# Kernel optimization log

Measured on AMD Instinct MI355X. Metric: run time of the kernel, lower is better.

Reference implementation:

```python
import jax, jax.numpy as jnp
import numpy as np

D_HIDDEN = 1024
NUM_HEADS = 16
D_HEAD = D_HIDDEN // NUM_HEADS


def setup_inputs() -> dict:
    key = jax.random.key(0)
    ks = jax.random.split(key, 9)
    N, S, D = 4, 2048, D_HIDDEN
    s = 1.0 / np.sqrt(D)
    inp = {
        "x": jax.random.normal(ks[0], (N, S, D), dtype=jnp.float32),
        "Wq": jax.random.uniform(ks[1], (D, D), jnp.float32, -s, s),
        "bq": jnp.zeros((D,), jnp.float32),
        "Wk": jax.random.uniform(ks[2], (D, D), jnp.float32, -s, s),
        "bk": jnp.zeros((D,), jnp.float32),
        "Wv": jax.random.uniform(ks[3], (D, D), jnp.float32, -s, s),
        "bv": jnp.zeros((D,), jnp.float32),
        "Wo": jax.random.uniform(ks[4], (D, D), jnp.float32, -s, s),
        "bo": jnp.zeros((D,), jnp.float32),
        "ln_gamma": jnp.ones((D,), jnp.float32),
        "ln_beta": jnp.zeros((D,), jnp.float32),
    }
    return inp


def _layer_norm(x, gamma, beta, eps=1e-5):
    mu = jnp.mean(x, axis=-1, keepdims=True)
    var = jnp.var(x, axis=-1, keepdims=True)
    return (x - mu) * jax.lax.rsqrt(var + eps) * gamma + beta


def reference(x, Wq, bq, Wk, bk, Wv, bv, Wo, bo, ln_gamma, ln_beta):
    N, S, D = x.shape
    H, Dh = NUM_HEADS, D_HEAD
    xn = _layer_norm(x, ln_gamma, ln_beta)
    # torch Linear: y = x @ W.T + b
    q = (xn @ Wq.T + bq).reshape(N, S, H, Dh)
    k = (xn @ Wk.T + bk).reshape(N, S, H, Dh)
    v = (xn @ Wv.T + bv).reshape(N, S, H, Dh)
    # scores: [N, H, S, S]
    scores = jnp.einsum('nxhd,nyhd->nhxy', q, k) / np.sqrt(Dh)
    # causal mask: positions y > x get -inf
    mask = jnp.triu(jnp.full((S, S), -jnp.inf, dtype=scores.dtype), k=1)
    attn = jax.nn.softmax(scores + mask[None, None], axis=-1)
    z = jnp.einsum('nhxy,nyhd->nxhd', attn, v).reshape(N, S, D)
    return z @ Wo.T + bo
```

## Files before the change

### kernel.cpp

```cpp
#include <hip/hip_runtime.h>

typedef unsigned short u16;
typedef unsigned int   u32;
typedef __bf16 bf16x8 __attribute__((ext_vector_type(8)));
typedef float  f32x4  __attribute__((ext_vector_type(4)));
typedef unsigned short u16x8 __attribute__((ext_vector_type(8)));
typedef unsigned short u16x4 __attribute__((ext_vector_type(4)));

#define SEQ 2048
#define DM  1024
#define TOKS 8388608
#define SCLQ 0.18033688f

__device__ __forceinline__ float bf2f(u16 u) {
    u32 i = ((u32)u) << 16;
    float f; __builtin_memcpy(&f, &i, 4); return f;
}
__device__ __forceinline__ u16 f2bf(float f) {
    u32 i; __builtin_memcpy(&i, &f, 4);
    return (u16)((i + 0x7FFFu + ((i >> 16) & 1u)) >> 16);
}
__device__ __forceinline__ bf16x8 ld8(const u16* p) {
    return __builtin_bit_cast(bf16x8, *(const u16x8*)p);
}
#define GLD16(src, dst) __builtin_amdgcn_global_load_lds( \
    (const __attribute__((address_space(1))) void*)(src), \
    (__attribute__((address_space(3))) void*)(dst), 16, 0, 0)

__global__ __launch_bounds__(64) void detect_k(const u32* __restrict__ x, int* __restrict__ flag) {
    const int lane = threadIdx.x;
    u32 w = x[lane];
    int e0 = (int)((w >> 7) & 0xFFu);
    int cnt = (e0 >= 100 && e0 <= 140) ? 1 : 0;
#pragma unroll
    for (int off = 32; off; off >>= 1) cnt += __shfl_xor(cnt, off);
    if (lane == 0) *flag = (cnt < 32) ? 1 : 0;
}

__global__ __launch_bounds__(256) void convert_k(const void* s0, const void* s1, const void* s2, const void* s3,
                                                 const void* v0, const void* v1, const void* v2, const void* v3,
                                                 const void* v4, const void* v5,
                                                 u16* __restrict__ dstW, u16* __restrict__ dstV,
                                                 const int* __restrict__ flagp) {
    const int y = blockIdx.y, tid = threadIdx.x;
    const int fp32m = *flagp;
    const void* src; u16* dst; size_t off;
    if (y < 4) {
        src = (y == 0) ? s0 : (y == 1) ? s1 : (y == 2) ? s2 : s3;
        dst = dstW + (size_t)y * 1048576;
        off = (size_t)blockIdx.x * 1024 + tid * 4;
    } else {
        const int i = blockIdx.x;
        if (i >= 6) return;
        src = (i == 0) ? v0 : (i == 1) ? v1 : (i == 2) ? v2 : (i == 3) ? v3 : (i == 4) ? v4 : v5;
        dst = dstV + (size_t)i * 1024;
        off = (size_t)tid * 4;
    }
    u16x4 o;
    if (fp32m) {
        const float* f = (const float*)src + off;
#pragma unroll
        for (int j = 0; j < 4; ++j) o[j] = f2bf(f[j]);
    } else {
        o = *(const u16x4*)((const u16*)src + off);
    }
    *(u16x4*)(dst + off) = o;
}

__global__ __launch_bounds__(256) void ln_k(const void* __restrict__ xv,
                                            const u16* __restrict__ g,
                                            const u16* __restrict__ b,
                                            u16* __restrict__ xn,
                                            const int* __restrict__ flagp) {
    const int row = blockIdx.x, tid = threadIdx.x;
    const int fp32m = *flagp;
    float f[4], s1 = 0.f, s2 = 0.f;
    if (fp32m) {
        f32x4 v = *(const f32x4*)((const float*)xv + (size_t)row * DM + tid * 4);
#pragma unroll
        for (int j = 0; j < 4; ++j) f[j] = v[j];
    } else {
        u16x4 v = *(const u16x4*)((const u16*)xv + (size_t)row * DM + tid * 4);
#pragma unroll
        for (int j = 0; j < 4; ++j) f[j] = bf2f(v[j]);
    }
#pragma unroll
    for (int j = 0; j < 4; ++j) { s1 += f[j]; s2 += f[j] * f[j]; }
#pragma unroll
    for (int off = 32; off; off >>= 1) { s1 += __shfl_xor(s1, off); s2 += __shfl_xor(s2, off); }
    __shared__ float red[8];
    const int wave = tid >> 6, lane = tid & 63;
    if (lane == 0) { red[wave] = s1; red[4 + wave] = s2; }
    __syncthreads();
    s1 = red[0] + red[1] + red[2] + red[3];
    s2 = red[4] + red[5] + red[6] + red[7];
    const float mu = s1 * (1.f / DM);
    const float var = s2 * (1.f / DM) - mu * mu;
    const float rs = rsqrtf(var + 1e-5f);
    u16x4 gv = *(const u16x4*)(g + tid * 4);
    u16x4 bv = *(const u16x4*)(b + tid * 4);
    u16x4 o;
#pragma unroll
    for (int j = 0; j < 4; ++j) o[j] = f2bf((f[j] - mu) * rs * bf2f(gv[j]) + bf2f(bv[j]));
    *(u16x4*)(xn + (size_t)row * DM + tid * 4) = o;
}

template <int VT>
__device__ __forceinline__ void gemm_core(u16* As, u16* Bs,
                                          const u16* __restrict__ A,
                                          const u16* __restrict__ W,
                                          const u16* __restrict__ bias,
                                          u16* __restrict__ out,
                                          const int* __restrict__ flagp,
                                          float scale) {
    const int tid = threadIdx.x, wave = tid >> 6, lane = tid & 63;
    const int l4 = lane & 15, q4 = lane >> 4;
    const int bm = blockIdx.x, bn = blockIdx.y;
    const int wm = (wave >> 1) * 64, wn = (wave & 1) * 64;
    int fp32m = 0;
    if (VT == 2) fp32m = *flagp;
    f32x4 acc[4][4] = {};
    const int srow = wave * 32 + (lane >> 2);
    const int skoff = (lane & 3) * 8;
    const u16* Ag = A + ((size_t)(bm * 128 + srow)) * DM + skoff;
    const u16* Wg = W + ((size_t)(bn * 128 + srow)) * DM + skoff;
    u16* As0 = As + wave * 1024;
    u16* Bs0 = Bs + wave * 1024;

    for (int k0 = 0; k0 < DM; k0 += 32) {
        GLD16(Ag + k0, As0);
        GLD16(Ag + 16 * DM + k0, As0 + 512);
        GLD16(Wg + k0, Bs0);
        GLD16(Wg + 16 * DM + k0, Bs0 + 512);
        __syncthreads();
        bf16x8 af[4], bfr[4];
#pragma unroll
        for (int t = 0; t < 4; ++t)
            af[t] = ld8(As + (wm + t * 16 + l4) * 32 + q4 * 8);
#pragma unroll
        for (int t = 0; t < 4; ++t)
            bfr[t] = ld8(Bs + (wn + t * 16 + l4) * 32 + q4 * 8);
#pragma unroll
        for (int mt = 0; mt < 4; ++mt)
#pragma unroll
            for (int nt = 0; nt < 4; ++nt)
                acc[mt][nt] = __builtin_amdgcn_mfma_f32_16x16x32_bf16(af[mt], bfr[nt], acc[mt][nt], 0, 0, 0);
        __syncthreads();
    }

#pragma unroll
    for (int nt = 0; nt < 4; ++nt) {
        const int col = bn * 128 + wn + nt * 16 + l4;
        const float bs = bf2f(bias[col]);
#pragma unroll
        for (int mt = 0; mt < 4; ++mt) {
            const int row0 = bm * 128 + wm + mt * 16 + q4 * 4;
            if (VT == 1) {
                const int nb = row0 >> 11, s0 = row0 & 2047;
                u16x4 pk;
#pragma unroll
                for (int r = 0; r < 4; ++r) pk[r] = f2bf((acc[mt][nt][r] + bs) * scale);
                *(u16x4*)(out + ((size_t)(nb * 1024 + col)) * SEQ + s0) = pk;
            } else if (VT == 2 && fp32m) {
#pragma unroll
                for (int r = 0; r < 4; ++r)
                    ((float*)out)[(size_t)(row0 + r) * DM + col] = acc[mt][nt][r] + bs;
            } else {
#pragma unroll
                for (int r = 0; r < 4; ++r)
                    out[(size_t)(row0 + r) * DM + col] = f2bf((acc[mt][nt][r] + bs) * scale);
            }
        }
    }
}

__global__ __launch_bounds__(256) void gemm_qkv_k(const u16* __restrict__ xn, const u16* __restrict__ Wc,
                                                  const u16* __restrict__ Vc,
                                                  u16* __restrict__ Q, u16* __restrict__ K, u16* __restrict__ Vt) {
    __shared__ alignas(16) u16 As[128 * 32];
    __shared__ alignas(16) u16 Bs[128 * 32];
    const int z = blockIdx.z;
    if (z == 0)      gemm_core<0>(As, Bs, xn, Wc,               Vc,        Q,  nullptr, SCLQ);
    else if (z == 1) gemm_core<0>(As, Bs, xn, Wc + 1048576,     Vc + 1024, K,  nullptr, 1.0f);
    else             gemm_core<1>(As, Bs, xn, Wc + 2 * 1048576, Vc + 2048, Vt, nullptr, 1.0f);
}

__global__ __launch_bounds__(256) void gemm_out_k(const u16* __restrict__ Z, const u16* __restrict__ Wc,
                                                  const u16* __restrict__ Vc,
                                                  u16* __restrict__ out, const int* __restrict__ flagp) {
    __shared__ alignas(16) u16 As[128 * 32];
    __shared__ alignas(16) u16 Bs[128 * 32];
    gemm_core<2>(As, Bs, Z, Wc + 3 * 1048576, Vc + 3 * 1024, out, flagp, 1.0f);
}

__global__ __launch_bounds__(256, 4) void flash_k(const u16* __restrict__ Q,
                                                  const u16* __restrict__ K,
                                                  const u16* __restrict__ Vt,
                                                  u16* __restrict__ Z) {
    const int bh = blockIdx.x;
    const int qb = 15 - (int)blockIdx.y;
    const int n = bh >> 4, h = bh & 15;
    const int tid = threadIdx.x, wave = tid >> 6, lane = tid & 63;
    const int l4 = lane & 15, q4 = lane >> 4;

    __shared__ alignas(16) u16 Ks[2][64 * 32];
    __shared__ alignas(16) u16 Vs[2][64 * 32];
    __shared__ alignas(16) u16 Pl[4][2][16 * 72];

    const int Q0w = qb * 128 + wave * 32;
    bf16x8 qf[2][2];
#pragma unroll
    for (int qt = 0; qt < 2; ++qt) {
        const u16* Qr = Q + ((size_t)(n * SEQ + Q0w + qt * 16 + l4)) * DM + h * 64 + q4 * 8;
        qf[qt][0] = ld8(Qr);
        qf[qt][1] = ld8(Qr + 32);
    }

    const int srow = lane >> 2, scol = (lane & 3) * 8;
    const u16* Kg = K + ((size_t)(n * SEQ + wave * 16 + srow)) * DM + h * 64 + scol;
    const u16* Vg = Vt + ((size_t)(n * 1024 + h * 64 + wave * 16 + srow)) * SEQ + scol;
    u16* KsD0 = &Ks[0][wave * 512];
    u16* KsD1 = &Ks[1][wave * 512];
    u16* VsD0 = &Vs[0][wave * 512];
    u16* VsD1 = &Vs[1][wave * 512];

    f32x4 o[2][4] = {};
    float l_acc[2] = {0.f, 0.f};
    const int nch = 2 * qb + 2;

    for (int c = 0; c < nch; ++c) {
        const int kv0 = c * 64;
        const size_t krow = (size_t)kv0 * DM;
        GLD16(Kg + krow, KsD0);
        GLD16(Kg + krow + 32, KsD1);
        GLD16(Vg + kv0, VsD0);
        GLD16(Vg + kv0 + 32, VsD1);
        __syncthreads();

        bf16x8 a[4][2];
#pragma unroll
        for (int mt = 0; mt < 4; ++mt) {
            a[mt][0] = ld8(&Ks[0][(mt * 16 + l4) * 32 + q4 * 8]);
            a[mt][1] = ld8(&Ks[1][(mt * 16 + l4) * 32 + q4 * 8]);
        }
#pragma unroll
        for (int qt = 0; qt < 2; ++qt) {
            f32x4 st[4];
#pragma unroll
            for (int mt = 0; mt < 4; ++mt) {
                f32x4 zz = {0.f, 0.f, 0.f, 0.f};
                st[mt] = __builtin_amdgcn_mfma_f32_16x16x32_bf16(a[mt][0], qf[qt][0], zz, 0, 0, 0);
                st[mt] = __builtin_amdgcn_mfma_f32_16x16x32_bf16(a[mt][1], qf[qt][1], st[mt], 0, 0, 0);
            }
            const int qg = Q0w + qt * 16 + l4;
            u16* P = Pl[wave][qt];
            float la = l_acc[qt];
#pragma unroll
            for (int mt = 0; mt < 4; ++mt) {
                __bf16 pk[4];
#pragma unroll
                for (int r = 0; r < 4; ++r) {
                    const int kv = kv0 + mt * 16 + q4 * 4 + r;
                    float p = __builtin_amdgcn_exp2f(st[mt][r]);
                    p = (kv > qg) ? 0.f : p;
                    la += p;
                    pk[r] = (__bf16)p;
                }
                *(u16x4*)(P + l4 * 72 + mt * 16 + q4 * 4) = *(u16x4*)pk;
            }
            l_acc[qt] = la;
        }
#pragma unroll
        for (int ks = 0; ks < 2; ++ks) {
            bf16x8 pf0 = ld8(&Pl[wave][0][l4 * 72 + ks * 32 + q4 * 8]);
            bf16x8 pf1 = ld8(&Pl[wave][1][l4 * 72 + ks * 32 + q4 * 8]);
#pragma unroll
            for (int nt = 0; nt < 4; ++nt) {
                bf16x8 vf = ld8(&Vs[ks][(nt * 16 + l4) * 32 + q4 * 8]);
                o[0][nt] = __builtin_amdgcn_mfma_f32_16x16x32_bf16(pf0, vf, o[0][nt], 0, 0, 0);
                o[1][nt] = __builtin_amdgcn_mfma_f32_16x16x32_bf16(pf1, vf, o[1][nt], 0, 0, 0);
            }
        }
        __syncthreads();
    }

#pragma unroll
    for (int qt = 0; qt < 2; ++qt) {
        float l = l_acc[qt];
        l += __shfl_xor(l, 16);
        l += __shfl_xor(l, 32);
        float lr[4];
#pragma unroll
        for (int r = 0; r < 4; ++r) lr[r] = 1.f / __shfl(l, q4 * 4 + r);
#pragma unroll
        for (int nt = 0; nt < 4; ++nt) {
            const int col = h * 64 + nt * 16 + l4;
#pragma unroll
            for (int r = 0; r < 4; ++r) {
                const int row = n * SEQ + Q0w + qt * 16 + q4 * 4 + r;
                Z[(size_t)row * DM + col] = f2bf(o[qt][nt][r] * lr[r]);
            }
        }
    }
}

extern "C" void kernel_launch(void* const* d_in, const int* in_sizes, int n_in,
                              void* d_out, int out_size, void* d_ws, size_t ws_size,
                              hipStream_t stream) {
    const void* x  = d_in[0];
    const void* Wq = d_in[1];
    const void* bq = d_in[2];
    const void* Wk = d_in[3];
    const void* bk = d_in[4];
    const void* Wv = d_in[5];
    const void* bv = d_in[6];
    const void* Wo = d_in[7];
    const void* bo = d_in[8];
    const void* g  = d_in[9];
    const void* b  = d_in[10];
    u16* ws = (u16*)d_ws;

    u16* xn  = ws;
    u16* Qb  = ws + (size_t)TOKS;
    u16* Kb  = ws + (size_t)2 * TOKS;
    u16* Vtb = ws + (size_t)3 * TOKS;
    u16* Zb  = ws;
    u16* Wc  = ws + (size_t)4 * TOKS;
    u16* Vc  = Wc + 4 * 1048576;
    int* flagp = (int*)(Vc + 8 * 1024);

    detect_k<<<dim3(1), 64, 0, stream>>>((const u32*)x, flagp);
    convert_k<<<dim3(1024, 5), 256, 0, stream>>>(Wq, Wk, Wv, Wo, bq, bk, bv, bo, g, b, Wc, Vc, flagp);
    ln_k<<<dim3(4 * SEQ), 256, 0, stream>>>(x, Vc + 4 * 1024, Vc + 5 * 1024, xn, flagp);
    gemm_qkv_k<<<dim3(64, 8, 3), 256, 0, stream>>>(xn, Wc, Vc, Qb, Kb, Vtb);
    flash_k<<<dim3(64, 16), 256, 0, stream>>>(Qb, Kb, Vtb, Zb);
    gemm_out_k<<<dim3(64, 8), 256, 0, stream>>>(Zb, Wc, Vc, (u16*)d_out, flagp);
}
```

Before: 256.6 us.

## Fuse detect, convert and layernorm into one prep kernel; widen output GEMM

Replaces the three launches for dtype detection, weight/bias conversion and layernorm with a single prep kernel. Each block sniffs the dtype itself, so no flag round-trip is needed, and layernorm reads gamma and beta directly from the source instead of from converted copies. This removes two launches and the serial dependence between them. The output projection GEMM now uses 512 threads, with half the waves loading A and half loading B, and each wave computes a 64x32 sub-tile to raise occupancy and parallelism. The trade-off is that every prep block redoes the dtype sniff.

```diff
diff --git a/kernel.cpp b/kernel.cpp
--- a/kernel.cpp
+++ b/kernel.cpp
@@ -27,82 +27,94 @@
     (const __attribute__((address_space(1))) void*)(src), \
     (__attribute__((address_space(3))) void*)(dst), 16, 0, 0)
 
-__global__ __launch_bounds__(64) void detect_k(const u32* __restrict__ x, int* __restrict__ flag) {
-    const int lane = threadIdx.x;
-    u32 w = x[lane];
+__device__ __forceinline__ int sniff_fp32(const u32* x) {
+    u32 w = x[threadIdx.x & 63];
     int e0 = (int)((w >> 7) & 0xFFu);
     int cnt = (e0 >= 100 && e0 <= 140) ? 1 : 0;
 #pragma unroll
     for (int off = 32; off; off >>= 1) cnt += __shfl_xor(cnt, off);
-    if (lane == 0) *flag = (cnt < 32) ? 1 : 0;
-}
-
-__global__ __launch_bounds__(256) void convert_k(const void* s0, const void* s1, const void* s2, const void* s3,
-                                                 const void* v0, const void* v1, const void* v2, const void* v3,
-                                                 const void* v4, const void* v5,
-                                                 u16* __restrict__ dstW, u16* __restrict__ dstV,
-                                                 const int* __restrict__ flagp) {
-    const int y = blockIdx.y, tid = threadIdx.x;
-    const int fp32m = *flagp;
-    const void* src; u16* dst; size_t off;
-    if (y < 4) {
-        src = (y == 0) ? s0 : (y == 1) ? s1 : (y == 2) ? s2 : s3;
-        dst = dstW + (size_t)y * 1048576;
-        off = (size_t)blockIdx.x * 1024 + tid * 4;
+    return cnt < 32;
+}
+
+__global__ __launch_bounds__(256) void prep_k(const void* __restrict__ x,
+                                              const void* Wq, const void* Wk, const void* Wv, const void* Wo,
+                                              const void* bq, const void* bk, const void* bv, const void* bo,
+                                              const void* g, const void* b,
+                                              u16* __restrict__ dstW, u16* __restrict__ dstV,
+                                              u16* __restrict__ xn, int* __restrict__ flagp) {
+    const int bid = blockIdx.x, tid = threadIdx.x;
+    const int fp32m = sniff_fp32((const u32*)x);
+
+    if (bid < 8192) {
+        const int row = bid;
+        float f[4], s1 = 0.f, s2 = 0.f;
+        if (fp32m) {
+            f32x4 v = *(const f32x4*)((const float*)x + (size_t)row * DM + tid * 4);
+#pragma unroll
+            for (int j = 0; j < 4; ++j) f[j] = v[j];
+        } else {
+            u16x4 v = *(const u16x4*)((const u16*)x + (size_t)row * DM + tid * 4);
+#pragma unroll
+            for (int j = 0; j < 4; ++j) f[j] = bf2f(v[j]);
+        }
+#pragma unroll
+        for (int j = 0; j < 4; ++j) { s1 += f[j]; s2 += f[j] * f[j]; }
+#pragma unroll
+        for (int off = 32; off; off >>= 1) { s1 += __shfl_xor(s1, off); s2 += __shfl_xor(s2, off); }
+        __shared__ float red[8];
+        const int wave = tid >> 6, lane = tid & 63;
+        if (lane == 0) { red[wave] = s1; red[4 + wave] = s2; }
+        __syncthreads();
+        s1 = red[0] + red[1] + red[2] + red[3];
+        s2 = red[4] + red[5] + red[6] + red[7];
+        const float mu = s1 * (1.f / DM);
+        const float var = s2 * (1.f / DM) - mu * mu;
+        const float rs = rsqrtf(var + 1e-5f);
+        float gv[4], bv2[4];
+        if (fp32m) {
+            f32x4 gg = *(const f32x4*)((const float*)g + tid * 4);
+            f32x4 bb = *(const f32x4*)((const float*)b + tid * 4);
+#pragma unroll
+            for (int j = 0; j < 4; ++j) { gv[j] = gg[j]; bv2[j] = bb[j]; }
+        } else {
+            u16x4 gg = *(const u16x4*)((const u16*)g + tid * 4);
+            u16x4 bb = *(const u16x4*)((const u16*)b + tid * 4);
+#pragma unroll
+            for (int j = 0; j < 4; ++j) { gv[j] = bf2f(gg[j]); bv2[j] = bf2f(bb[j]); }
+        }
+        u16x4 o;
+#pragma unroll
+        for (int j = 0; j < 4; ++j) o[j] = f2bf((f[j] - mu) * rs * gv[j] + bv2[j]);
+        *(u16x4*)(xn + (size_t)row * DM + tid * 4) = o;
+    } else if (bid < 12288) {
+        const int wi = (bid - 8192) >> 10, blk = (bid - 8192) & 1023;
+        const void* src = (wi == 0) ? Wq : (wi == 1) ? Wk : (wi == 2) ? Wv : Wo;
+        const size_t off = (size_t)blk * 1024 + tid * 4;
+        u16x4 o;
+        if (fp32m) {
+            const float* f = (const float*)src + off;
+#pragma unroll
+            for (int j = 0; j < 4; ++j) o[j] = f2bf(f[j]);
+        } else {
+            o = *(const u16x4*)((const u16*)src + off);
+        }
+        *(u16x4*)(dstW + (size_t)wi * 1048576 + off) = o;
     } else {
-        const int i = blockIdx.x;
-        if (i >= 6) return;
-        src = (i == 0) ? v0 : (i == 1) ? v1 : (i == 2) ? v2 : (i == 3) ? v3 : (i == 4) ? v4 : v5;
-        dst = dstV + (size_t)i * 1024;
-        off = (size_t)tid * 4;
-    }
-    u16x4 o;
-    if (fp32m) {
-        const float* f = (const float*)src + off;
-#pragma unroll
-        for (int j = 0; j < 4; ++j) o[j] = f2bf(f[j]);
-    } else {
-        o = *(const u16x4*)((const u16*)src + off);
-    }
-    *(u16x4*)(dst + off) = o;
-}
-
-__global__ __launch_bounds__(256) void ln_k(const void* __restrict__ xv,
-                                            const u16* __restrict__ g,
-                                            const u16* __restrict__ b,
-                                            u16* __restrict__ xn,
-                                            const int* __restrict__ flagp) {
-    const int row = blockIdx.x, tid = threadIdx.x;
-    const int fp32m = *flagp;
-    float f[4], s1 = 0.f, s2 = 0.f;
-    if (fp32m) {
-        f32x4 v = *(const f32x4*)((const float*)xv + (size_t)row * DM + tid * 4);
-#pragma unroll
-        for (int j = 0; j < 4; ++j) f[j] = v[j];
-    } else {
-        u16x4 v = *(const u16x4*)((const u16*)xv + (size_t)row * DM + tid * 4);
-#pragma unroll
-        for (int j = 0; j < 4; ++j) f[j] = bf2f(v[j]);
-    }
-#pragma unroll
-    for (int j = 0; j < 4; ++j) { s1 += f[j]; s2 += f[j] * f[j]; }
-#pragma unroll
-    for (int off = 32; off; off >>= 1) { s1 += __shfl_xor(s1, off); s2 += __shfl_xor(s2, off); }
-    __shared__ float red[8];
-    const int wave = tid >> 6, lane = tid & 63;
-    if (lane == 0) { red[wave] = s1; red[4 + wave] = s2; }
-    __syncthreads();
-    s1 = red[0] + red[1] + red[2] + red[3];
-    s2 = red[4] + red[5] + red[6] + red[7];
-    const float mu = s1 * (1.f / DM);
-    const float var = s2 * (1.f / DM) - mu * mu;
-    const float rs = rsqrtf(var + 1e-5f);
-    u16x4 gv = *(const u16x4*)(g + tid * 4);
-    u16x4 bv = *(const u16x4*)(b + tid * 4);
-    u16x4 o;
-#pragma unroll
-    for (int j = 0; j < 4; ++j) o[j] = f2bf((f[j] - mu) * rs * bf2f(gv[j]) + bf2f(bv[j]));
-    *(u16x4*)(xn + (size_t)row * DM + tid * 4) = o;
+#pragma unroll
+        for (int i = 0; i < 4; ++i) {
+            const void* src = (i == 0) ? bq : (i == 1) ? bk : (i == 2) ? bv : bo;
+            u16x4 o;
+            if (fp32m) {
+                const float* f = (const float*)src + tid * 4;
+#pragma unroll
+                for (int j = 0; j < 4; ++j) o[j] = f2bf(f[j]);
+            } else {
+                o = *(const u16x4*)((const u16*)src + tid * 4);
+            }
+            *(u16x4*)(dstV + (size_t)i * 1024 + tid * 4) = o;
+        }
+        if (tid == 0) *flagp = fp32m;
+    }
 }
 
 template <int VT>
@@ -111,14 +123,11 @@
                                           const u16* __restrict__ W,
                                           const u16* __restrict__ bias,
                                           u16* __restrict__ out,
-                                          const int* __restrict__ flagp,
                                           float scale) {
     const int tid = threadIdx.x, wave = tid >> 6, lane = tid & 63;
     const int l4 = lane & 15, q4 = lane >> 4;
     const int bm = blockIdx.x, bn = blockIdx.y;
     const int wm = (wave >> 1) * 64, wn = (wave & 1) * 64;
-    int fp32m = 0;
-    if (VT == 2) fp32m = *flagp;
     f32x4 acc[4][4] = {};
     const int srow = wave * 32 + (lane >> 2);
     const int skoff = (lane & 3) * 8;
@@ -161,10 +170,6 @@
 #pragma unroll
                 for (int r = 0; r < 4; ++r) pk[r] = f2bf((acc[mt][nt][r] + bs) * scale);
                 *(u16x4*)(out + ((size_t)(nb * 1024 + col)) * SEQ + s0) = pk;
-            } else if (VT == 2 && fp32m) {
-#pragma unroll
-                for (int r = 0; r < 4; ++r)
-                    ((float*)out)[(size_t)(row0 + r) * DM + col] = acc[mt][nt][r] + bs;
             } else {
 #pragma unroll
                 for (int r = 0; r < 4; ++r)
@@ -180,17 +185,67 @@
     __shared__ alignas(16) u16 As[128 * 32];
     __shared__ alignas(16) u16 Bs[128 * 32];
     const int z = blockIdx.z;
-    if (z == 0)      gemm_core<0>(As, Bs, xn, Wc,               Vc,        Q,  nullptr, SCLQ);
-    else if (z == 1) gemm_core<0>(As, Bs, xn, Wc + 1048576,     Vc + 1024, K,  nullptr, 1.0f);
-    else             gemm_core<1>(As, Bs, xn, Wc + 2 * 1048576, Vc + 2048, Vt, nullptr, 1.0f);
-}
-
-__global__ __launch_bounds__(256) void gemm_out_k(const u16* __restrict__ Z, const u16* __restrict__ Wc,
+    if (z == 0)      gemm_core<0>(As, Bs, xn, Wc,               Vc,        Q,  SCLQ);
+    else if (z == 1) gemm_core<0>(As, Bs, xn, Wc + 1048576,     Vc + 1024, K,  1.0f);
+    else             gemm_core<1>(As, Bs, xn, Wc + 2 * 1048576, Vc + 2048, Vt, 1.0f);
+}
+
+__global__ __launch_bounds__(512) void gemm_out_k(const u16* __restrict__ Z, const u16* __restrict__ Wc,
                                                   const u16* __restrict__ Vc,
                                                   u16* __restrict__ out, const int* __restrict__ flagp) {
     __shared__ alignas(16) u16 As[128 * 32];
     __shared__ alignas(16) u16 Bs[128 * 32];
-    gemm_core<2>(As, Bs, Z, Wc + 3 * 1048576, Vc + 3 * 1024, out, flagp, 1.0f);
+    const u16* W = Wc + 3 * 1048576;
+    const u16* bias = Vc + 3 * 1024;
+    const int tid = threadIdx.x, wave = tid >> 6, lane = tid & 63;
+    const int l4 = lane & 15, q4 = lane >> 4;
+    const int bm = blockIdx.x, bn = blockIdx.y;
+    const int wm = (wave >> 2) * 64, wn = (wave & 3) * 32;
+    const int fp32m = *flagp;
+    f32x4 acc[4][2] = {};
+    const int srow = (wave & 3) * 32 + (lane >> 2);
+    const int skoff = (lane & 3) * 8;
+    const u16* Sg = (wave < 4) ? (Z + ((size_t)(bm * 128 + srow)) * DM + skoff)
+                               : (W + ((size_t)(bn * 128 + srow)) * DM + skoff);
+    u16* dst0 = (wave < 4) ? (As + (wave & 3) * 1024) : (Bs + (wave & 3) * 1024);
+
+    for (int k0 = 0; k0 < DM; k0 += 32) {
+        GLD16(Sg + k0, dst0);
+        GLD16(Sg + 16 * DM + k0, dst0 + 512);
+        __syncthreads();
+        bf16x8 af[4], bfr[2];
+#pragma unroll
+        for (int t = 0; t < 4; ++t)
+            af[t] = ld8(As + (wm + t * 16 + l4) * 32 + q4 * 8);
+#pragma unroll
+        for (int t = 0; t < 2; ++t)
+            bfr[t] = ld8(Bs + (wn + t * 16 + l4) * 32 + q4 * 8);
+#pragma unroll
+        for (int mt = 0; mt < 4; ++mt)
+#pragma unroll
+            for (int nt = 0; nt < 2; ++nt)
+                acc[mt][nt] = __builtin_amdgcn_mfma_f32_16x16x32_bf16(af[mt], bfr[nt], acc[mt][nt], 0, 0, 0);
+        __syncthreads();
+    }
+
+#pragma unroll
+    for (int nt = 0; nt < 2; ++nt) {
+        const int col = bn * 128 + wn + nt * 16 + l4;
+        const float bs = bf2f(bias[col]);
+#pragma unroll
+        for (int mt = 0; mt < 4; ++mt) {
+            const int row0 = bm * 128 + wm + mt * 16 + q4 * 4;
+            if (fp32m) {
+#pragma unroll
+                for (int r = 0; r < 4; ++r)
+                    ((float*)out)[(size_t)(row0 + r) * DM + col] = acc[mt][nt][r] + bs;
+            } else {
+#pragma unroll
+                for (int r = 0; r < 4; ++r)
+                    out[(size_t)(row0 + r) * DM + col] = f2bf(acc[mt][nt][r] + bs);
+            }
+        }
+    }
 }
 
 __global__ __launch_bounds__(256, 4) void flash_k(const u16* __restrict__ Q,
@@ -329,10 +384,8 @@
     u16* Vc  = Wc + 4 * 1048576;
     int* flagp = (int*)(Vc + 8 * 1024);
 
-    detect_k<<<dim3(1), 64, 0, stream>>>((const u32*)x, flagp);
-    convert_k<<<dim3(1024, 5), 256, 0, stream>>>(Wq, Wk, Wv, Wo, bq, bk, bv, bo, g, b, Wc, Vc, flagp);
-    ln_k<<<dim3(4 * SEQ), 256, 0, stream>>>(x, Vc + 4 * 1024, Vc + 5 * 1024, xn, flagp);
+    prep_k<<<dim3(12289), 256, 0, stream>>>(x, Wq, Wk, Wv, Wo, bq, bk, bv, bo, g, b, Wc, Vc, xn, flagp);
     gemm_qkv_k<<<dim3(64, 8, 3), 256, 0, stream>>>(xn, Wc, Vc, Qb, Kb, Vtb);
     flash_k<<<dim3(64, 16), 256, 0, stream>>>(Qb, Kb, Vtb, Zb);
-    gemm_out_k<<<dim3(64, 8), 256, 0, stream>>>(Zb, Wc, Vc, (u16*)d_out, flagp);
-}
+    gemm_out_k<<<dim3(64, 8), 512, 0, stream>>>(Zb, Wc, Vc, (u16*)d_out, flagp);
+}
```

Result: no change. 259.4 us (+1.1%).
